# Kernel optimization log

Hardware: AMD Instinct MI355X
Metric: run time of the kernel (lower is better)

Reference implementation:

```python
import jax, jax.numpy as jnp
import numpy as np

B, T, D_MODEL, HEAD = 8, 2048, 1024, 64
NEG = -1e9  # finite mask fill; exp underflows to 0 in softmax, avoids inf/NaN


def setup_inputs() -> dict:
    key = jax.random.key(0)
    k1, k2, k3, k4, k5 = jax.random.split(key, 5)
    x = jax.random.normal(k1, (B, T, D_MODEL), dtype=jnp.float32)
    valid_lens = jax.random.randint(k2, (B,), 0, T)
    # nn.Linear(d_model, head_size, bias=False): y = x @ W, W: (d_model, head_size)
    s = 0.02
    Wq = jax.random.normal(k3, (D_MODEL, HEAD), dtype=jnp.float32) * s
    Wk = jax.random.normal(k4, (D_MODEL, HEAD), dtype=jnp.float32) * s
    Wv = jax.random.normal(k5, (D_MODEL, HEAD), dtype=jnp.float32) * s
    return {"x": x, "Wq": Wq, "Wk": Wk, "Wv": Wv, "valid_lens": valid_lens}


def reference(x, Wq, Wk, Wv, valid_lens):
    # x: (B, T, D), projections -> (B, T, H)
    q = jnp.einsum("btd,dh->bth", x, Wq)
    k = jnp.einsum("btd,dh->bth", x, Wk)
    v = jnp.einsum("btd,dh->bth", x, Wv)
    scale = k.shape[-1] ** -0.5
    wei = jnp.einsum("bqh,bkh->bqk", q, k) * scale  # (B, T, T)

    t = jnp.arange(T)
    causal = t[None, :] <= t[:, None]                     # (T, T) lower-tri
    valid = t[None, :] < valid_lens[:, None]              # (B, T)
    mask = causal[None, :, :] & valid[:, :, None] & valid[:, None, :]  # (B, T, T)

    wei = jnp.where(mask, wei, NEG)
    attn = jax.nn.softmax(wei, axis=2)
    # rows with no valid key get all-masked scores -> original code zeros them out
    row_all_masked = ~jnp.any(mask, axis=2)               # (B, T)
    attn = jnp.where(row_all_masked[:, :, None], 0.0, attn)
    # dropout(p=0.0) == identity
    out = jnp.einsum("bqk,bkh->bqh", attn, v)             # (B, T, H)
    return out
```

## Files before the change

### kernel.cpp

```cpp
#include <hip/hip_runtime.h>
#include <hip/hip_bf16.h>
#include <stdint.h>

#define T_   2048
#define DM_  1024
#define HD_  64
#define NROW 16384

typedef __attribute__((ext_vector_type(8))) __bf16 bf16x8;
typedef __attribute__((ext_vector_type(4))) __bf16 bf16x4;
typedef __attribute__((ext_vector_type(4))) float  f32x4;

__global__ void wconv_k(const float* __restrict__ Wq, const float* __restrict__ Wk,
                        const float* __restrict__ Wv, __bf16* __restrict__ wfrag) {
    int tid  = blockIdx.x * 256 + threadIdx.x;
    int lane = tid & 63;
    int t    = (tid >> 6) % 12;
    int kc   = tid / (12 * 64);
    int c = lane & 15, g = lane >> 4;
    int n = t * 16 + c;
    const float* W = (n < 64) ? Wq : (n < 128) ? Wk : Wv;
    int col = n & 63;
    int k0  = kc * 32 + g * 8;
    __bf16* dst = wfrag + (size_t)tid * 8;
#pragma unroll
    for (int j = 0; j < 8; ++j) dst[j] = (__bf16)W[(k0 + j) * HD_ + col];
}

__global__ __launch_bounds__(256) void proj_k(const float* __restrict__ x,
        const __bf16* __restrict__ wfrag, __bf16* __restrict__ Qb,
        __bf16* __restrict__ Kb, __bf16* __restrict__ Vt) {
    int lane = threadIdx.x & 63, wave = threadIdx.x >> 6;
    int c = lane & 15, g = lane >> 4;
    int row0 = blockIdx.x * 64 + wave * 16;
    const float* xp = x + (size_t)(row0 + c) * DM_ + g * 8;
    f32x4 acc[12];
#pragma unroll
    for (int t = 0; t < 12; ++t) acc[t] = (f32x4)0.f;
    for (int kc = 0; kc < 32; ++kc) {
        const f32x4* ap = (const f32x4*)(xp + kc * 32);
        f32x4 a0 = ap[0], a1 = ap[1];
        bf16x8 af;
#pragma unroll
        for (int j = 0; j < 4; ++j) { af[j] = (__bf16)a0[j]; af[j + 4] = (__bf16)a1[j]; }
        const bf16x8* bp = (const bf16x8*)(wfrag + (size_t)kc * 12 * 512);
#pragma unroll
        for (int t = 0; t < 12; ++t) {
            bf16x8 bf = bp[t * 64 + lane];
            acc[t] = __builtin_amdgcn_mfma_f32_16x16x32_bf16(af, bf, acc[t], 0, 0, 0);
        }
    }
#pragma unroll
    for (int t = 0; t < 12; ++t) {
        int w    = t >> 2;
        int ncol = (t & 3) * 16 + c;
#pragma unroll
        for (int r = 0; r < 4; ++r) {
            int grow = row0 + g * 4 + r;
            float v  = acc[t][r];
            if (w == 0)      Qb[(size_t)grow * HD_ + ncol] = (__bf16)(v * 0.125f);
            else if (w == 1) Kb[(size_t)grow * HD_ + ncol] = (__bf16)v;
            else             Vt[(size_t)(grow >> 11) * (HD_ * T_) + (size_t)ncol * T_ + (grow & 2047)] = (__bf16)v;
        }
    }
}

__global__ __launch_bounds__(128) void attn_k(const __bf16* __restrict__ Qb,
        const __bf16* __restrict__ Kb, const __bf16* __restrict__ Vt,
        const int* __restrict__ vlen, float* __restrict__ out) {
    int bid  = blockIdx.x;
    int half = bid >> 8, idx = bid & 255;
    int b = idx >> 5, p = idx & 31;
    int qb = half ? (63 - p) : p;
    int wave = threadIdx.x >> 6, lane = threadIdx.x & 63;
    int c = lane & 15, g = lane >> 4;
    int qg = qb * 32 + wave * 16 + c;
    const __bf16* qp = Qb + (size_t)(b * T_ + qg) * HD_ + g * 8;
    bf16x8 qf0 = *(const bf16x8*)qp;
    bf16x8 qf1 = *(const bf16x8*)(qp + 32);
    const __bf16* Kbase = Kb + (size_t)b * T_ * HD_;
    const __bf16* Vbase = Vt + (size_t)b * HD_ * T_;
    f32x4 o0 = (f32x4)0.f, o1 = (f32x4)0.f, o2 = (f32x4)0.f, o3 = (f32x4)0.f;
    float m = -1e30f, lsum = 0.f;
    __shared__ __bf16 plds[2][16][40];
    __bf16 (*pl)[40] = plds[wave];
    int numT = qb + 1;
    for (int kt = 0; kt < numT; ++kt) {
        int kv0 = kt * 32;
        const __bf16* kp = Kbase + (size_t)(kv0 + c) * HD_ + g * 8;
        bf16x8 k00 = *(const bf16x8*)kp;
        bf16x8 k01 = *(const bf16x8*)(kp + 32);
        bf16x8 k10 = *(const bf16x8*)(kp + 16 * HD_);
        bf16x8 k11 = *(const bf16x8*)(kp + 16 * HD_ + 32);
        f32x4 s0 = (f32x4)0.f, s1 = (f32x4)0.f;
        s0 = __builtin_amdgcn_mfma_f32_16x16x32_bf16(k00, qf0, s0, 0, 0, 0);
        s0 = __builtin_amdgcn_mfma_f32_16x16x32_bf16(k01, qf1, s0, 0, 0, 0);
        s1 = __builtin_amdgcn_mfma_f32_16x16x32_bf16(k10, qf0, s1, 0, 0, 0);
        s1 = __builtin_amdgcn_mfma_f32_16x16x32_bf16(k11, qf1, s1, 0, 0, 0);
        float s[8];
#pragma unroll
        for (int r = 0; r < 4; ++r) { s[r] = s0[r]; s[4 + r] = s1[r]; }
        if (kt == numT - 1) {
#pragma unroll
            for (int i = 0; i < 8; ++i) {
                int kv = kv0 + (i >> 2) * 16 + g * 4 + (i & 3);
                if (kv > qg) s[i] = -1e30f;
            }
        }
        float tm = s[0];
#pragma unroll
        for (int i = 1; i < 8; ++i) tm = fmaxf(tm, s[i]);
        tm = fmaxf(tm, __shfl_xor(tm, 16));
        tm = fmaxf(tm, __shfl_xor(tm, 32));
        float mn = fmaxf(m, tm);
        float al = __expf(m - mn);
        float ps = 0.f;
#pragma unroll
        for (int i = 0; i < 8; ++i) { s[i] = __expf(s[i] - mn); ps += s[i]; }
        ps += __shfl_xor(ps, 16);
        ps += __shfl_xor(ps, 32);
        lsum = lsum * al + ps;
        m = mn;
        o0 *= al; o1 *= al; o2 *= al; o3 *= al;
        bf16x4 p0, p1;
#pragma unroll
        for (int r = 0; r < 4; ++r) { p0[r] = (__bf16)s[r]; p1[r] = (__bf16)s[4 + r]; }
        *(bf16x4*)&pl[c][g * 4]      = p0;
        *(bf16x4*)&pl[c][16 + g * 4] = p1;
        bf16x8 pf = *(const bf16x8*)&pl[c][g * 8];
        const __bf16* vp = Vbase + (size_t)c * T_ + kv0 + g * 8;
        bf16x8 v0 = *(const bf16x8*)(vp);
        bf16x8 v1 = *(const bf16x8*)(vp + 16 * T_);
        bf16x8 v2 = *(const bf16x8*)(vp + 32 * T_);
        bf16x8 v3 = *(const bf16x8*)(vp + 48 * T_);
        o0 = __builtin_amdgcn_mfma_f32_16x16x32_bf16(v0, pf, o0, 0, 0, 0);
        o1 = __builtin_amdgcn_mfma_f32_16x16x32_bf16(v1, pf, o1, 0, 0, 0);
        o2 = __builtin_amdgcn_mfma_f32_16x16x32_bf16(v2, pf, o2, 0, 0, 0);
        o3 = __builtin_amdgcn_mfma_f32_16x16x32_bf16(v3, pf, o3, 0, 0, 0);
    }
    float inv  = 1.f / lsum;
    bool  dead = (qg >= vlen[b]);
    float* op  = out + (size_t)(b * T_ + qg) * HD_ + g * 4;
    f32x4 r0 = dead ? (f32x4)0.f : o0 * inv;
    f32x4 r1 = dead ? (f32x4)0.f : o1 * inv;
    f32x4 r2 = dead ? (f32x4)0.f : o2 * inv;
    f32x4 r3 = dead ? (f32x4)0.f : o3 * inv;
    *(f32x4*)(op)      = r0;
    *(f32x4*)(op + 16) = r1;
    *(f32x4*)(op + 32) = r2;
    *(f32x4*)(op + 48) = r3;
}

extern "C" void kernel_launch(void* const* d_in, const int* in_sizes, int n_in,
                              void* d_out, int out_size, void* d_ws, size_t ws_size,
                              hipStream_t stream) {
    const float* x   = (const float*)d_in[0];
    const float* Wq  = (const float*)d_in[1];
    const float* Wk  = (const float*)d_in[2];
    const float* Wv  = (const float*)d_in[3];
    const int*   vln = (const int*)d_in[4];
    float* out = (float*)d_out;

    __bf16* Qb    = (__bf16*)d_ws;
    __bf16* Kb    = Qb + (size_t)NROW * HD_;
    __bf16* Vt    = Kb + (size_t)NROW * HD_;
    __bf16* wfrag = Vt + (size_t)NROW * HD_;

    wconv_k<<<96, 256, 0, stream>>>(Wq, Wk, Wv, wfrag);
    proj_k <<<256, 256, 0, stream>>>(x, wfrag, Qb, Kb, Vt);
    attn_k <<<512, 128, 0, stream>>>(Qb, Kb, Vt, vln, out);
}
```

Measured before the change: 177.3 us.

## Split projection across Q/K/V blocks and widen attention KV tile to 64

```diff
diff --git a/kernel.cpp b/kernel.cpp
--- a/kernel.cpp
+++ b/kernel.cpp
@@ -31,36 +31,37 @@
         const __bf16* __restrict__ wfrag, __bf16* __restrict__ Qb,
         __bf16* __restrict__ Kb, __bf16* __restrict__ Vt) {
     int lane = threadIdx.x & 63, wave = threadIdx.x >> 6;
+    int ng = blockIdx.x >> 8;
+    int rt = blockIdx.x & 255;
     int c = lane & 15, g = lane >> 4;
-    int row0 = blockIdx.x * 64 + wave * 16;
+    int row0 = rt * 64 + wave * 16;
     const float* xp = x + (size_t)(row0 + c) * DM_ + g * 8;
-    f32x4 acc[12];
+    f32x4 acc[4];
 #pragma unroll
-    for (int t = 0; t < 12; ++t) acc[t] = (f32x4)0.f;
+    for (int t = 0; t < 4; ++t) acc[t] = (f32x4)0.f;
     for (int kc = 0; kc < 32; ++kc) {
         const f32x4* ap = (const f32x4*)(xp + kc * 32);
         f32x4 a0 = ap[0], a1 = ap[1];
         bf16x8 af;
 #pragma unroll
         for (int j = 0; j < 4; ++j) { af[j] = (__bf16)a0[j]; af[j + 4] = (__bf16)a1[j]; }
-        const bf16x8* bp = (const bf16x8*)(wfrag + (size_t)kc * 12 * 512);
+        const bf16x8* bp = (const bf16x8*)(wfrag + (size_t)kc * 12 * 512) + ng * 256;
 #pragma unroll
-        for (int t = 0; t < 12; ++t) {
+        for (int t = 0; t < 4; ++t) {
             bf16x8 bf = bp[t * 64 + lane];
             acc[t] = __builtin_amdgcn_mfma_f32_16x16x32_bf16(af, bf, acc[t], 0, 0, 0);
         }
     }
 #pragma unroll
-    for (int t = 0; t < 12; ++t) {
-        int w    = t >> 2;
-        int ncol = (t & 3) * 16 + c;
+    for (int t = 0; t < 4; ++t) {
+        int ncol = t * 16 + c;
 #pragma unroll
         for (int r = 0; r < 4; ++r) {
             int grow = row0 + g * 4 + r;
             float v  = acc[t][r];
-            if (w == 0)      Qb[(size_t)grow * HD_ + ncol] = (__bf16)(v * 0.125f);
-            else if (w == 1) Kb[(size_t)grow * HD_ + ncol] = (__bf16)v;
-            else             Vt[(size_t)(grow >> 11) * (HD_ * T_) + (size_t)ncol * T_ + (grow & 2047)] = (__bf16)v;
+            if (ng == 0)      Qb[(size_t)grow * HD_ + ncol] = (__bf16)(v * 0.125f);
+            else if (ng == 1) Kb[(size_t)grow * HD_ + ncol] = (__bf16)v;
+            else              Vt[(size_t)(grow >> 11) * (HD_ * T_) + (size_t)ncol * T_ + (grow & 2047)] = (__bf16)v;
         }
     }
 }
@@ -82,61 +83,82 @@
     const __bf16* Vbase = Vt + (size_t)b * HD_ * T_;
     f32x4 o0 = (f32x4)0.f, o1 = (f32x4)0.f, o2 = (f32x4)0.f, o3 = (f32x4)0.f;
     float m = -1e30f, lsum = 0.f;
-    __shared__ __bf16 plds[2][16][40];
-    __bf16 (*pl)[40] = plds[wave];
-    int numT = qb + 1;
-    for (int kt = 0; kt < numT; ++kt) {
-        int kv0 = kt * 32;
+    __shared__ __bf16 plds[2][16][72];
+    __bf16 (*pl)[72] = plds[wave];
+    int nd2 = (qb + 2) >> 1;
+    for (int kt = 0; kt < nd2; ++kt) {
+        int kv0 = kt * 64;
         const __bf16* kp = Kbase + (size_t)(kv0 + c) * HD_ + g * 8;
-        bf16x8 k00 = *(const bf16x8*)kp;
-        bf16x8 k01 = *(const bf16x8*)(kp + 32);
-        bf16x8 k10 = *(const bf16x8*)(kp + 16 * HD_);
-        bf16x8 k11 = *(const bf16x8*)(kp + 16 * HD_ + 32);
-        f32x4 s0 = (f32x4)0.f, s1 = (f32x4)0.f;
-        s0 = __builtin_amdgcn_mfma_f32_16x16x32_bf16(k00, qf0, s0, 0, 0, 0);
-        s0 = __builtin_amdgcn_mfma_f32_16x16x32_bf16(k01, qf1, s0, 0, 0, 0);
-        s1 = __builtin_amdgcn_mfma_f32_16x16x32_bf16(k10, qf0, s1, 0, 0, 0);
-        s1 = __builtin_amdgcn_mfma_f32_16x16x32_bf16(k11, qf1, s1, 0, 0, 0);
-        float s[8];
+        bf16x8 ka00 = *(const bf16x8*)(kp);
+        bf16x8 ka01 = *(const bf16x8*)(kp + 32);
+        bf16x8 ka10 = *(const bf16x8*)(kp + 16 * HD_);
+        bf16x8 ka11 = *(const bf16x8*)(kp + 16 * HD_ + 32);
+        bf16x8 kb00 = *(const bf16x8*)(kp + 32 * HD_);
+        bf16x8 kb01 = *(const bf16x8*)(kp + 32 * HD_ + 32);
+        bf16x8 kb10 = *(const bf16x8*)(kp + 48 * HD_);
+        bf16x8 kb11 = *(const bf16x8*)(kp + 48 * HD_ + 32);
+        f32x4 sa0 = (f32x4)0.f, sa1 = (f32x4)0.f, sb0 = (f32x4)0.f, sb1 = (f32x4)0.f;
+        sa0 = __builtin_amdgcn_mfma_f32_16x16x32_bf16(ka00, qf0, sa0, 0, 0, 0);
+        sa0 = __builtin_amdgcn_mfma_f32_16x16x32_bf16(ka01, qf1, sa0, 0, 0, 0);
+        sa1 = __builtin_amdgcn_mfma_f32_16x16x32_bf16(ka10, qf0, sa1, 0, 0, 0);
+        sa1 = __builtin_amdgcn_mfma_f32_16x16x32_bf16(ka11, qf1, sa1, 0, 0, 0);
+        sb0 = __builtin_amdgcn_mfma_f32_16x16x32_bf16(kb00, qf0, sb0, 0, 0, 0);
+        sb0 = __builtin_amdgcn_mfma_f32_16x16x32_bf16(kb01, qf1, sb0, 0, 0, 0);
+        sb1 = __builtin_amdgcn_mfma_f32_16x16x32_bf16(kb10, qf0, sb1, 0, 0, 0);
+        sb1 = __builtin_amdgcn_mfma_f32_16x16x32_bf16(kb11, qf1, sb1, 0, 0, 0);
+        float s[16];
 #pragma unroll
-        for (int r = 0; r < 4; ++r) { s[r] = s0[r]; s[4 + r] = s1[r]; }
-        if (kt == numT - 1) {
+        for (int r = 0; r < 4; ++r) {
+            s[r] = sa0[r]; s[4 + r] = sa1[r]; s[8 + r] = sb0[r]; s[12 + r] = sb1[r];
+        }
+        if (kt == nd2 - 1) {
 #pragma unroll
-            for (int i = 0; i < 8; ++i) {
+            for (int i = 0; i < 16; ++i) {
                 int kv = kv0 + (i >> 2) * 16 + g * 4 + (i & 3);
                 if (kv > qg) s[i] = -1e30f;
             }
         }
         float tm = s[0];
 #pragma unroll
-        for (int i = 1; i < 8; ++i) tm = fmaxf(tm, s[i]);
+        for (int i = 1; i < 16; ++i) tm = fmaxf(tm, s[i]);
         tm = fmaxf(tm, __shfl_xor(tm, 16));
         tm = fmaxf(tm, __shfl_xor(tm, 32));
         float mn = fmaxf(m, tm);
         float al = __expf(m - mn);
         float ps = 0.f;
 #pragma unroll
-        for (int i = 0; i < 8; ++i) { s[i] = __expf(s[i] - mn); ps += s[i]; }
+        for (int i = 0; i < 16; ++i) { s[i] = __expf(s[i] - mn); ps += s[i]; }
         ps += __shfl_xor(ps, 16);
         ps += __shfl_xor(ps, 32);
         lsum = lsum * al + ps;
         m = mn;
         o0 *= al; o1 *= al; o2 *= al; o3 *= al;
-        bf16x4 p0, p1;
 #pragma unroll
-        for (int r = 0; r < 4; ++r) { p0[r] = (__bf16)s[r]; p1[r] = (__bf16)s[4 + r]; }
-        *(bf16x4*)&pl[c][g * 4]      = p0;
-        *(bf16x4*)&pl[c][16 + g * 4] = p1;
-        bf16x8 pf = *(const bf16x8*)&pl[c][g * 8];
+        for (int mt = 0; mt < 4; ++mt) {
+            bf16x4 pv;
+#pragma unroll
+            for (int r = 0; r < 4; ++r) pv[r] = (__bf16)s[mt * 4 + r];
+            *(bf16x4*)&pl[c][mt * 16 + g * 4] = pv;
+        }
+        bf16x8 pf0 = *(const bf16x8*)&pl[c][g * 8];
+        bf16x8 pf1 = *(const bf16x8*)&pl[c][32 + g * 8];
         const __bf16* vp = Vbase + (size_t)c * T_ + kv0 + g * 8;
-        bf16x8 v0 = *(const bf16x8*)(vp);
-        bf16x8 v1 = *(const bf16x8*)(vp + 16 * T_);
-        bf16x8 v2 = *(const bf16x8*)(vp + 32 * T_);
-        bf16x8 v3 = *(const bf16x8*)(vp + 48 * T_);
-        o0 = __builtin_amdgcn_mfma_f32_16x16x32_bf16(v0, pf, o0, 0, 0, 0);
-        o1 = __builtin_amdgcn_mfma_f32_16x16x32_bf16(v1, pf, o1, 0, 0, 0);
-        o2 = __builtin_amdgcn_mfma_f32_16x16x32_bf16(v2, pf, o2, 0, 0, 0);
-        o3 = __builtin_amdgcn_mfma_f32_16x16x32_bf16(v3, pf, o3, 0, 0, 0);
+        bf16x8 v0a = *(const bf16x8*)(vp);
+        bf16x8 v1a = *(const bf16x8*)(vp + 16 * T_);
+        bf16x8 v2a = *(const bf16x8*)(vp + 32 * T_);
+        bf16x8 v3a = *(const bf16x8*)(vp + 48 * T_);
+        bf16x8 v0b = *(const bf16x8*)(vp + 32);
+        bf16x8 v1b = *(const bf16x8*)(vp + 16 * T_ + 32);
+        bf16x8 v2b = *(const bf16x8*)(vp + 32 * T_ + 32);
+        bf16x8 v3b = *(const bf16x8*)(vp + 48 * T_ + 32);
+        o0 = __builtin_amdgcn_mfma_f32_16x16x32_bf16(v0a, pf0, o0, 0, 0, 0);
+        o1 = __builtin_amdgcn_mfma_f32_16x16x32_bf16(v1a, pf0, o1, 0, 0, 0);
+        o2 = __builtin_amdgcn_mfma_f32_16x16x32_bf16(v2a, pf0, o2, 0, 0, 0);
+        o3 = __builtin_amdgcn_mfma_f32_16x16x32_bf16(v3a, pf0, o3, 0, 0, 0);
+        o0 = __builtin_amdgcn_mfma_f32_16x16x32_bf16(v0b, pf1, o0, 0, 0, 0);
+        o1 = __builtin_amdgcn_mfma_f32_16x16x32_bf16(v1b, pf1, o1, 0, 0, 0);
+        o2 = __builtin_amdgcn_mfma_f32_16x16x32_bf16(v2b, pf1, o2, 0, 0, 0);
+        o3 = __builtin_amdgcn_mfma_f32_16x16x32_bf16(v3b, pf1, o3, 0, 0, 0);
     }
     float inv  = 1.f / lsum;
     bool  dead = (qg >= vlen[b]);
@@ -167,6 +189,6 @@
     __bf16* wfrag = Vt + (size_t)NROW * HD_;
 
     wconv_k<<<96, 256, 0, stream>>>(Wq, Wk, Wv, wfrag);
-    proj_k <<<256, 256, 0, stream>>>(x, wfrag, Qb, Kb, Vt);
+    proj_k <<<768, 256, 0, stream>>>(x, wfrag, Qb, Kb, Vt);
     attn_k <<<512, 128, 0, stream>>>(Qb, Kb, Vt, vln, out);
 }
```

New measurement: 175.4 us. About the same (-1.0%).
